# Kernel tuning notes

Measured on AMD Instinct MI355X. Metric: run time of the kernel, lower is better.

The kernel has to match this reference:

```python
import jax, jax.numpy as jnp
import numpy as np

N_ATOMS = 100000
M_NBRS = 12
ATOM_F = 64
NBR_F = 41
BN_EPS = 1e-5


def setup_inputs() -> dict:
    key = jax.random.key(0)
    k1, k2, k3, k4, k5 = jax.random.split(key, 5)
    atom_fea = jax.random.normal(k1, (N_ATOMS, ATOM_F), dtype=jnp.float32)
    nbr_fea = jax.random.normal(k2, (N_ATOMS, M_NBRS, NBR_F), dtype=jnp.float32)
    # fc_full: Linear(2*atom + nbr -> 2*atom), torch layout [out, in]
    in_dim = 2 * ATOM_F + NBR_F
    out_dim = 2 * ATOM_F
    W = jax.random.normal(k3, (out_dim, in_dim), dtype=jnp.float32) * (1.0 / np.sqrt(in_dim))
    b = jax.random.normal(k4, (out_dim,), dtype=jnp.float32) * 0.01
    gamma = jnp.ones((ATOM_F,), dtype=jnp.float32)
    beta = jnp.zeros((ATOM_F,), dtype=jnp.float32)
    nbr_idx = jax.random.randint(k5, (N_ATOMS, M_NBRS), 0, N_ATOMS, dtype=jnp.int32)
    return {"atom_fea": atom_fea, "nbr_fea": nbr_fea, "W": W, "b": b,
            "gamma": gamma, "beta": beta, "nbr_idx": nbr_idx}


def reference(atom_fea, nbr_fea, W, b, gamma, beta, nbr_idx):
    N, M = nbr_idx.shape
    F = atom_fea.shape[1]
    # gather neighbor atom features: [N, M, F]
    nbr_atom_fea = atom_fea[nbr_idx]
    # broadcast self features: [N, M, F]
    self_fea = jnp.broadcast_to(atom_fea[:, None, :], (N, M, F))
    # concat [self, nbr_atom, edge] -> [N, M, 2F + nbr_F]
    total_fea = jnp.concatenate([self_fea, nbr_atom_fea, nbr_fea], axis=2)
    # shared linear: [N, M, 2F]
    total_fea = jnp.einsum('nmi,oi->nmo', total_fea, W) + b
    filter_fea, core_fea = jnp.split(total_fea, 2, axis=2)
    # gated message, sum over neighbors -> [N, F]
    nbr_msg = (jax.nn.sigmoid(filter_fea) * jax.nn.softplus(core_fea)).sum(axis=1)
    # BatchNorm1d (training mode: batch stats, biased variance)
    x = atom_fea + nbr_msg
    mean = x.mean(axis=0)
    var = x.var(axis=0)
    x_hat = (x - mean) * jax.lax.rsqrt(var + BN_EPS)
    out = x_hat * gamma + beta
    return jax.nn.softplus(out)
```

## Files before the change

### kernel.cpp

```cpp
#include <hip/hip_runtime.h>

#define N_ATOMS 100000
#define M_NBRS 12
#define ATOM_F 64
#define NBR_F 41
#define OUT_DIM 128
#define IN_DIM 169
#define N_GROUPS (N_ATOMS / 16)
#define LOG2E 1.44269504f
#define LN2   0.69314718f

typedef __attribute__((ext_vector_type(8))) short short8;
typedef __attribute__((ext_vector_type(4))) float f32x4;
typedef __attribute__((ext_vector_type(4))) unsigned u32x4;

__device__ __forceinline__ unsigned cvt_pk(float a, float b) {
    unsigned r;
    asm("v_cvt_pk_bf16_f32 %0, %1, %2" : "=v"(r) : "v"(a), "v"(b));
    return r;
}
__device__ __forceinline__ float fexp2(float x) { return __builtin_amdgcn_exp2f(x); }
__device__ __forceinline__ float flog2(float x) { return __builtin_amdgcn_logf(x); }
__device__ __forceinline__ float frcp(float x)  { return __builtin_amdgcn_rcpf(x); }
__device__ __forceinline__ float softplus_f(float x) {
    return fmaxf(x, 0.f) + __logf(1.f + __expf(-fabsf(x)));
}

__global__ __launch_bounds__(256, 4) void k_prep(
    const float* __restrict__ atom, const float* __restrict__ W,
    const float* __restrict__ bias, unsigned* __restrict__ abf_u32,
    unsigned* __restrict__ A1P, float* __restrict__ SUM)
{
    __shared__ __align__(16) unsigned BFp[16 * 64 * 4];
    const int tid = threadIdx.x;
    const int w = tid >> 6, l = tid & 63;
    const int r = l & 15, g = l >> 4;

    if (blockIdx.x == 0 && tid < 128) SUM[tid] = 0.f;

    #pragma unroll
    for (int s = 0; s < 4; ++s) {
        int f = s * 4 + w;
        int nt = f >> 1, kk = f & 1;
        int col = nt * 16 + r;
        int kbase = kk * 32 + g * 8;
        const float* wp = W + col * IN_DIM + kbase;
        u32x4 pk;
        pk[0] = cvt_pk(wp[0] * LOG2E, wp[1] * LOG2E);
        pk[1] = cvt_pk(wp[2] * LOG2E, wp[3] * LOG2E);
        pk[2] = cvt_pk(wp[4] * LOG2E, wp[5] * LOG2E);
        pk[3] = cvt_pk(wp[6] * LOG2E, wp[7] * LOG2E);
        *reinterpret_cast<u32x4*>(&BFp[(f * 64 + l) * 4]) = pk;
    }
    __syncthreads();

    const int gw = blockIdx.x * 4 + w;
    if (gw >= N_GROUPS) return;
    const int base = gw * 16;

    float bb[8];
    #pragma unroll
    for (int nt = 0; nt < 8; ++nt) bb[nt] = bias[nt * 16 + r] * LOG2E;

    union { u32x4 u; short8 s; } af[2];
    #pragma unroll
    for (int kk = 0; kk < 2; ++kk) {
        const float4* ap = reinterpret_cast<const float4*>(atom)
                           + (size_t)(base + r) * 16 + kk * 8 + g * 2;
        float4 v0 = ap[0], v1 = ap[1];
        af[kk].u[0] = cvt_pk(v0.x, v0.y); af[kk].u[1] = cvt_pk(v0.z, v0.w);
        af[kk].u[2] = cvt_pk(v1.x, v1.y); af[kk].u[3] = cvt_pk(v1.z, v1.w);
        *reinterpret_cast<u32x4*>(&abf_u32[(size_t)(base + r) * 32 + kk * 16 + g * 4])
            = af[kk].u;
    }

    u32x4 outp[4];
    #pragma unroll
    for (int nt = 0; nt < 4; ++nt) {
        f32x4 accf = {0.f,0.f,0.f,0.f}, accc = {0.f,0.f,0.f,0.f};
        #pragma unroll
        for (int kk = 0; kk < 2; ++kk) {
            union { u32x4 u; short8 s; } uf, uc;
            uf.u = *reinterpret_cast<const u32x4*>(&BFp[((nt * 2 + kk) * 64 + l) * 4]);
            uc.u = *reinterpret_cast<const u32x4*>(&BFp[(((nt + 4) * 2 + kk) * 64 + l) * 4]);
            accf = __builtin_amdgcn_mfma_f32_16x16x32_bf16(af[kk].s, uf.s, accf, 0,0,0);
            accc = __builtin_amdgcn_mfma_f32_16x16x32_bf16(af[kk].s, uc.s, accc, 0,0,0);
        }
        #pragma unroll
        for (int r4 = 0; r4 < 4; ++r4)
            outp[r4][nt] = cvt_pk(accf[r4] + bb[nt], accc[r4] + bb[nt + 4]);
    }
    #pragma unroll
    for (int r4 = 0; r4 < 4; ++r4)
        *reinterpret_cast<u32x4*>(&A1P[(size_t)gw * 1024 + r4 * 256 + l * 4]) = outp[r4];
}

struct EBuf { unsigned p2[4]; unsigned p3[4]; };

__device__ __forceinline__ EBuf load_edges(const float* __restrict__ ep, int g)
{
    EBuf b;
    f32x4 v0, v1;
    __builtin_memcpy(&v0, ep + g * 8, 16);
    __builtin_memcpy(&v1, ep + g * 8 + 4, 16);
    b.p2[0] = cvt_pk(v0[0], v0[1]); b.p2[1] = cvt_pk(v0[2], v0[3]);
    b.p2[2] = cvt_pk(v1[0], v1[1]); b.p2[3] = cvt_pk(v1[2], v1[3]);
    b.p3[0] = b.p3[1] = b.p3[2] = b.p3[3] = 0u;
    if (g == 0) {
        f32x4 u0, u1;
        __builtin_memcpy(&u0, ep + 32, 16);
        __builtin_memcpy(&u1, ep + 36, 16);
        b.p3[0] = cvt_pk(u0[0], u0[1]); b.p3[1] = cvt_pk(u0[2], u0[3]);
        b.p3[2] = cvt_pk(u1[0], u1[1]); b.p3[3] = cvt_pk(u1[2], u1[3]);
    } else if (g == 1) {
        b.p3[0] = cvt_pk(ep[40], 0.f);
    }
    return b;
}

__global__ __launch_bounds__(256, 4) void k_msg(
    const float* __restrict__ atom, const float* __restrict__ nbr,
    const float* __restrict__ W, const int* __restrict__ idx,
    const unsigned* __restrict__ abf, const unsigned* __restrict__ A1P,
    float* __restrict__ X, float* __restrict__ SUM)
{
    __shared__ __align__(16) unsigned BF[32 * 64 * 4];
    const int tid = threadIdx.x;
    const int w = tid >> 6, l = tid & 63;
    const int c = l & 15, g = l >> 4;

    #pragma unroll
    for (int s = 0; s < 8; ++s) {
        int f = s * 4 + w;
        int nt = f >> 2, kk = f & 3;
        int col = nt * 16 + c;
        int kbase = kk * 32 + g * 8;
        const float* wp = W + col * IN_DIM + 64 + kbase;
        u32x4 pk;
        float v[8];
        #pragma unroll
        for (int j = 0; j < 8; ++j)
            v[j] = (kbase + j < 105) ? wp[j] * LOG2E : 0.f;
        pk[0] = cvt_pk(v[0], v[1]); pk[1] = cvt_pk(v[2], v[3]);
        pk[2] = cvt_pk(v[4], v[5]); pk[3] = cvt_pk(v[6], v[7]);
        *reinterpret_cast<u32x4*>(&BF[(f * 64 + l) * 4]) = pk;
    }
    __syncthreads();

    const int gw = blockIdx.x * 4 + w;
    float sum_p[4] = {0.f,0.f,0.f,0.f}, sq_p[4] = {0.f,0.f,0.f,0.f};

    if (gw < N_GROUPS) {
        const int base = gw * 16;
        u32x4 a1q[4];
        #pragma unroll
        for (int r4 = 0; r4 < 4; ++r4)
            a1q[r4] = *reinterpret_cast<const u32x4*>(
                &A1P[(size_t)gw * 1024 + r4 * 256 + l * 4]);

        float gs[4][4];
        #pragma unroll
        for (int r4 = 0; r4 < 4; ++r4)
          #pragma unroll
          for (int p = 0; p < 4; ++p) gs[r4][p] = 0.f;

        const int irow = (base + c) * M_NBRS;
        const float* erow = nbr + (size_t)irow * NBR_F;

        unsigned bofs = (unsigned)l * 16u;

        u32x4 at0, at1, at0n, at1n;
        EBuf eb, ebn;
        int jn;
        {
            int j0 = idx[irow];
            at0 = *reinterpret_cast<const u32x4*>(abf + (size_t)j0 * 32 + g * 4);
            at1 = *reinterpret_cast<const u32x4*>(abf + (size_t)j0 * 32 + 16 + g * 4);
            eb = load_edges(erow, g);
        }
        jn = idx[irow + 1];

        #pragma unroll 1
        for (int m = 0; m < M_NBRS; ++m) {
            if (m + 1 < M_NBRS) {
                at0n = *reinterpret_cast<const u32x4*>(abf + (size_t)jn * 32 + g * 4);
                at1n = *reinterpret_cast<const u32x4*>(abf + (size_t)jn * 32 + 16 + g * 4);
                ebn = load_edges(erow + (m + 1) * NBR_F, g);
                if (m + 2 < M_NBRS) jn = idx[irow + m + 2];
            }
            asm volatile("" : "+v"(bofs));
            const char* bsb = reinterpret_cast<const char*>(BF);
            union { u32x4 u; short8 s; } a0, a1, a2, a3;
            a0.u = at0; a1.u = at1;
            a2.u[0] = eb.p2[0]; a2.u[1] = eb.p2[1]; a2.u[2] = eb.p2[2]; a2.u[3] = eb.p2[3];
            a3.u[0] = eb.p3[0]; a3.u[1] = eb.p3[1]; a3.u[2] = eb.p3[2]; a3.u[3] = eb.p3[3];
            #pragma unroll
            for (int p = 0; p < 4; ++p) {
                f32x4 accf, accc;
                #pragma unroll
                for (int r4 = 0; r4 < 4; ++r4) {
                    unsigned v = a1q[r4][p];
                    accf[r4] = __uint_as_float(v << 16);
                    accc[r4] = __uint_as_float(v & 0xffff0000u);
                }
                #pragma unroll
                for (int kk = 0; kk < 4; ++kk) {
                    union { u32x4 u; short8 s; } uf, uc;
                    uf.u = *reinterpret_cast<const u32x4*>(
                        bsb + bofs + (unsigned)((p * 4 + kk) * 64 * 16));
                    uc.u = *reinterpret_cast<const u32x4*>(
                        bsb + bofs + (unsigned)(((p + 4) * 4 + kk) * 64 * 16));
                    short8 afk = (kk == 0) ? a0.s : (kk == 1) ? a1.s
                               : (kk == 2) ? a2.s : a3.s;
                    accf = __builtin_amdgcn_mfma_f32_16x16x32_bf16(afk, uf.s, accf, 0,0,0);
                    accc = __builtin_amdgcn_mfma_f32_16x16x32_bf16(afk, uc.s, accc, 0,0,0);
                }
                #pragma unroll
                for (int r4 = 0; r4 < 4; ++r4) {
                    float sig = frcp(1.f + fexp2(-accf[r4]));
                    float sp  = flog2(1.f + fexp2(accc[r4])) * LN2;
                    gs[r4][p] += sig * sp;
                }
            }
            at0 = at0n; at1 = at1n; eb = ebn;
        }
        #pragma unroll
        for (int r4 = 0; r4 < 4; ++r4) {
            int o = (base + g * 4 + r4) * ATOM_F + c;
            #pragma unroll
            for (int p = 0; p < 4; ++p) {
                float x = atom[o + p * 16] + gs[r4][p];
                X[o + p * 16] = x;
                sum_p[p] += x;
                sq_p[p] += x * x;
            }
        }
    }

    #pragma unroll
    for (int p = 0; p < 4; ++p) {
        sum_p[p] += __shfl_xor(sum_p[p], 16, 64);
        sum_p[p] += __shfl_xor(sum_p[p], 32, 64);
        sq_p[p]  += __shfl_xor(sq_p[p], 16, 64);
        sq_p[p]  += __shfl_xor(sq_p[p], 32, 64);
    }
    __syncthreads();
    float* Rs = reinterpret_cast<float*>(BF);
    if (g == 0) {
        #pragma unroll
        for (int p = 0; p < 4; ++p) {
            Rs[w * 128 + p * 16 + c] = sum_p[p];
            Rs[512 + w * 128 + p * 16 + c] = sq_p[p];
        }
    }
    __syncthreads();
    if (tid < 128) {
        int q = tid & 63;
        int o = (tid >> 6) * 512;
        float v = Rs[o + q] + Rs[o + 128 + q] + Rs[o + 256 + q] + Rs[o + 384 + q];
        atomicAdd(&SUM[tid], v);
    }
}

__global__ void k_final(float* __restrict__ X, const float* __restrict__ SUM,
                        const float* __restrict__ gamma, const float* __restrict__ beta)
{
    int q = blockIdx.x * 256 + threadIdx.x;
    int fb = (q & 15);
    const float4* S4 = reinterpret_cast<const float4*>(SUM);
    float4 s1 = S4[fb];
    float4 s2 = S4[16 + fb];
    float4 gm = reinterpret_cast<const float4*>(gamma)[fb];
    float4 bt = reinterpret_cast<const float4*>(beta)[fb];
    const float inv_n = 1.f / N_ATOMS;
    float4 x = reinterpret_cast<const float4*>(X)[q];
    float4 o;
    {
        float mean = s1.x * inv_n, msq = s2.x * inv_n;
        float sc = rsqrtf(msq - mean * mean + 1e-5f) * gm.x;
        o.x = softplus_f(x.x * sc + (bt.x - mean * sc));
    }
    {
        float mean = s1.y * inv_n, msq = s2.y * inv_n;
        float sc = rsqrtf(msq - mean * mean + 1e-5f) * gm.y;
        o.y = softplus_f(x.y * sc + (bt.y - mean * sc));
    }
    {
        float mean = s1.z * inv_n, msq = s2.z * inv_n;
        float sc = rsqrtf(msq - mean * mean + 1e-5f) * gm.z;
        o.z = softplus_f(x.z * sc + (bt.z - mean * sc));
    }
    {
        float mean = s1.w * inv_n, msq = s2.w * inv_n;
        float sc = rsqrtf(msq - mean * mean + 1e-5f) * gm.w;
        o.w = softplus_f(x.w * sc + (bt.w - mean * sc));
    }
    reinterpret_cast<float4*>(X)[q] = o;
}

extern "C" void kernel_launch(void* const* d_in, const int* in_sizes, int n_in,
                              void* d_out, int out_size, void* d_ws, size_t ws_size,
                              hipStream_t stream)
{
    const float* atom  = (const float*)d_in[0];
    const float* nbr   = (const float*)d_in[1];
    const float* W     = (const float*)d_in[2];
    const float* bias  = (const float*)d_in[3];
    const float* gamma = (const float*)d_in[4];
    const float* beta  = (const float*)d_in[5];
    const int*   idx   = (const int*)d_in[6];
    float* X = (float*)d_out;

    char* ws = (char*)d_ws;
    unsigned* abf = (unsigned*)ws;
    unsigned* A1P = (unsigned*)(ws + (size_t)N_ATOMS * 32 * 4);
    float* SUM    = (float*)(ws + (size_t)N_ATOMS * 32 * 4
                                + (size_t)N_GROUPS * 1024 * 4);

    const int blocks = (N_GROUPS + 3) / 4;
    hipLaunchKernelGGL(k_prep,  dim3(blocks), dim3(256), 0, stream, atom, W, bias, abf, A1P, SUM);
    hipLaunchKernelGGL(k_msg,   dim3(blocks), dim3(256), 0, stream, atom, nbr, W, idx, abf, A1P, X, SUM);
    hipLaunchKernelGGL(k_final, dim3(6250),   dim3(256), 0, stream, X, SUM, gamma, beta);
}
```

Baseline: 415.9 us.

## Pre-convert edge features to padded bf16 neighbor-major buffer in prep kernel

Moves the fp32-to-bf16 conversion of the edge features out of the message kernel into the prep kernel. The prep kernel writes them as 96-byte padded rows laid out neighbor-slab by atom, so the message loop fetches each operand with two aligned 16-byte loads instead of unaligned fp32 loads plus converts. The cost is an extra pass that reads all edge features (about 197 MB of fp32) and writes a roughly 115 MB bf16 buffer, which is then read again. Each thread in the prep pass also does strided 164-byte row reads, which coalesce poorly. Overall global traffic likely goes up.

```diff
diff --git a/kernel.cpp b/kernel.cpp
--- a/kernel.cpp
+++ b/kernel.cpp
@@ -27,9 +27,10 @@
 }
 
 __global__ __launch_bounds__(256, 4) void k_prep(
-    const float* __restrict__ atom, const float* __restrict__ W,
-    const float* __restrict__ bias, unsigned* __restrict__ abf_u32,
-    unsigned* __restrict__ A1P, float* __restrict__ SUM)
+    const float* __restrict__ atom, const float* __restrict__ nbr,
+    const float* __restrict__ W, const float* __restrict__ bias,
+    unsigned* __restrict__ abf_u32, unsigned* __restrict__ A1P,
+    unsigned* __restrict__ EP, float* __restrict__ SUM)
 {
     __shared__ __align__(16) unsigned BFp[16 * 64 * 4];
     const int tid = threadIdx.x;
@@ -54,6 +55,26 @@
     }
     __syncthreads();
 
+    {
+        const int tot = N_ATOMS * M_NBRS;
+        const int stride = gridDim.x * 256;
+        for (int T = blockIdx.x * 256 + tid; T < tot; T += stride) {
+            int m = T - (T / M_NBRS) * M_NBRS;
+            int a = T / M_NBRS;
+            const float* ip = nbr + (size_t)T * NBR_F;
+            unsigned o[24];
+            #pragma unroll
+            for (int u = 0; u < 20; ++u) o[u] = cvt_pk(ip[2 * u], ip[2 * u + 1]);
+            o[20] = cvt_pk(ip[40], 0.f);
+            o[21] = 0u; o[22] = 0u; o[23] = 0u;
+            unsigned* op = EP + ((size_t)m * N_ATOMS + a) * 24;
+            #pragma unroll
+            for (int q = 0; q < 6; ++q)
+                *reinterpret_cast<u32x4*>(op + q * 4) =
+                    *reinterpret_cast<const u32x4*>(&o[q * 4]);
+        }
+    }
+
     const int gw = blockIdx.x * 4 + w;
     if (gw >= N_GROUPS) return;
     const int base = gw * 16;
@@ -95,33 +116,10 @@
         *reinterpret_cast<u32x4*>(&A1P[(size_t)gw * 1024 + r4 * 256 + l * 4]) = outp[r4];
 }
 
-struct EBuf { unsigned p2[4]; unsigned p3[4]; };
-
-__device__ __forceinline__ EBuf load_edges(const float* __restrict__ ep, int g)
-{
-    EBuf b;
-    f32x4 v0, v1;
-    __builtin_memcpy(&v0, ep + g * 8, 16);
-    __builtin_memcpy(&v1, ep + g * 8 + 4, 16);
-    b.p2[0] = cvt_pk(v0[0], v0[1]); b.p2[1] = cvt_pk(v0[2], v0[3]);
-    b.p2[2] = cvt_pk(v1[0], v1[1]); b.p2[3] = cvt_pk(v1[2], v1[3]);
-    b.p3[0] = b.p3[1] = b.p3[2] = b.p3[3] = 0u;
-    if (g == 0) {
-        f32x4 u0, u1;
-        __builtin_memcpy(&u0, ep + 32, 16);
-        __builtin_memcpy(&u1, ep + 36, 16);
-        b.p3[0] = cvt_pk(u0[0], u0[1]); b.p3[1] = cvt_pk(u0[2], u0[3]);
-        b.p3[2] = cvt_pk(u1[0], u1[1]); b.p3[3] = cvt_pk(u1[2], u1[3]);
-    } else if (g == 1) {
-        b.p3[0] = cvt_pk(ep[40], 0.f);
-    }
-    return b;
-}
-
 __global__ __launch_bounds__(256, 4) void k_msg(
-    const float* __restrict__ atom, const float* __restrict__ nbr,
-    const float* __restrict__ W, const int* __restrict__ idx,
-    const unsigned* __restrict__ abf, const unsigned* __restrict__ A1P,
+    const float* __restrict__ atom, const float* __restrict__ W,
+    const int* __restrict__ idx, const unsigned* __restrict__ abf,
+    const unsigned* __restrict__ A1P, const unsigned* __restrict__ EP,
     float* __restrict__ X, float* __restrict__ SUM)
 {
     __shared__ __align__(16) unsigned BF[32 * 64 * 4];
@@ -165,18 +163,21 @@
           for (int p = 0; p < 4; ++p) gs[r4][p] = 0.f;
 
         const int irow = (base + c) * M_NBRS;
-        const float* erow = nbr + (size_t)irow * NBR_F;
+        const char* EPb = reinterpret_cast<const char*>(EP);
+        const size_t e2off = (size_t)(base + c) * 96 + (size_t)g * 16;
+        const size_t e3off = (size_t)(base + c) * 96 + 64 + (g == 1 ? 16 : 0);
+        const size_t slab = (size_t)N_ATOMS * 96;
 
         unsigned bofs = (unsigned)l * 16u;
 
-        u32x4 at0, at1, at0n, at1n;
-        EBuf eb, ebn;
+        u32x4 at0, at1, at0n, at1n, e2, e3, e2n, e3n;
         int jn;
         {
             int j0 = idx[irow];
             at0 = *reinterpret_cast<const u32x4*>(abf + (size_t)j0 * 32 + g * 4);
             at1 = *reinterpret_cast<const u32x4*>(abf + (size_t)j0 * 32 + 16 + g * 4);
-            eb = load_edges(erow, g);
+            e2 = *reinterpret_cast<const u32x4*>(EPb + e2off);
+            e3 = *reinterpret_cast<const u32x4*>(EPb + e3off);
         }
         jn = idx[irow + 1];
 
@@ -185,15 +186,14 @@
             if (m + 1 < M_NBRS) {
                 at0n = *reinterpret_cast<const u32x4*>(abf + (size_t)jn * 32 + g * 4);
                 at1n = *reinterpret_cast<const u32x4*>(abf + (size_t)jn * 32 + 16 + g * 4);
-                ebn = load_edges(erow + (m + 1) * NBR_F, g);
+                e2n = *reinterpret_cast<const u32x4*>(EPb + (m + 1) * slab + e2off);
+                e3n = *reinterpret_cast<const u32x4*>(EPb + (m + 1) * slab + e3off);
                 if (m + 2 < M_NBRS) jn = idx[irow + m + 2];
             }
             asm volatile("" : "+v"(bofs));
             const char* bsb = reinterpret_cast<const char*>(BF);
             union { u32x4 u; short8 s; } a0, a1, a2, a3;
-            a0.u = at0; a1.u = at1;
-            a2.u[0] = eb.p2[0]; a2.u[1] = eb.p2[1]; a2.u[2] = eb.p2[2]; a2.u[3] = eb.p2[3];
-            a3.u[0] = eb.p3[0]; a3.u[1] = eb.p3[1]; a3.u[2] = eb.p3[2]; a3.u[3] = eb.p3[3];
+            a0.u = at0; a1.u = at1; a2.u = e2; a3.u = e3;
             #pragma unroll
             for (int p = 0; p < 4; ++p) {
                 f32x4 accf, accc;
@@ -222,7 +222,7 @@
                     gs[r4][p] += sig * sp;
                 }
             }
-            at0 = at0n; at1 = at1n; eb = ebn;
+            at0 = at0n; at1 = at1n; e2 = e2n; e3 = e3n;
         }
         #pragma unroll
         for (int r4 = 0; r4 < 4; ++r4) {
@@ -314,11 +314,16 @@
     char* ws = (char*)d_ws;
     unsigned* abf = (unsigned*)ws;
     unsigned* A1P = (unsigned*)(ws + (size_t)N_ATOMS * 32 * 4);
+    unsigned* EP  = (unsigned*)(ws + (size_t)N_ATOMS * 32 * 4
+                                   + (size_t)N_GROUPS * 1024 * 4);
     float* SUM    = (float*)(ws + (size_t)N_ATOMS * 32 * 4
-                                + (size_t)N_GROUPS * 1024 * 4);
+                                + (size_t)N_GROUPS * 1024 * 4
+                                + (size_t)N_ATOMS * M_NBRS * 24 * 4);
 
     const int blocks = (N_GROUPS + 3) / 4;
-    hipLaunchKernelGGL(k_prep,  dim3(blocks), dim3(256), 0, stream, atom, W, bias, abf, A1P, SUM);
-    hipLaunchKernelGGL(k_msg,   dim3(blocks), dim3(256), 0, stream, atom, nbr, W, idx, abf, A1P, X, SUM);
+    hipLaunchKernelGGL(k_prep,  dim3(blocks), dim3(256), 0, stream,
+                       atom, nbr, W, bias, abf, A1P, EP, SUM);
+    hipLaunchKernelGGL(k_msg,   dim3(blocks), dim3(256), 0, stream,
+                       atom, W, idx, abf, A1P, EP, X, SUM);
     hipLaunchKernelGGL(k_final, dim3(6250),   dim3(256), 0, stream, X, SUM, gamma, beta);
 }
```

After: 450.9 us. +8.4%, slower.

## Fuse self-feature projection into message kernel and deepen edge prefetch

Applied to the files above, without the earlier changes.

Moves the self-atom half of the linear layer (the A1P precompute) out of the prep kernel and into the message kernel, which computes it with MFMA straight into registers. This removes the A1P workspace write and re-read. It also deepens the edge-feature prefetch to two neighbors ahead to hide more global load latency. The cost is an extra LDS weight staging pass and barrier in k_msg, plus higher register pressure from the extra edge buffer.

```diff
diff --git a/kernel.cpp b/kernel.cpp
--- a/kernel.cpp
+++ b/kernel.cpp
@@ -27,72 +27,29 @@
 }
 
 __global__ __launch_bounds__(256, 4) void k_prep(
-    const float* __restrict__ atom, const float* __restrict__ W,
-    const float* __restrict__ bias, unsigned* __restrict__ abf_u32,
-    unsigned* __restrict__ A1P, float* __restrict__ SUM)
-{
-    __shared__ __align__(16) unsigned BFp[16 * 64 * 4];
+    const float* __restrict__ atom, unsigned* __restrict__ abf_u32,
+    float* __restrict__ SUM)
+{
     const int tid = threadIdx.x;
     const int w = tid >> 6, l = tid & 63;
     const int r = l & 15, g = l >> 4;
 
     if (blockIdx.x == 0 && tid < 128) SUM[tid] = 0.f;
 
-    #pragma unroll
-    for (int s = 0; s < 4; ++s) {
-        int f = s * 4 + w;
-        int nt = f >> 1, kk = f & 1;
-        int col = nt * 16 + r;
-        int kbase = kk * 32 + g * 8;
-        const float* wp = W + col * IN_DIM + kbase;
-        u32x4 pk;
-        pk[0] = cvt_pk(wp[0] * LOG2E, wp[1] * LOG2E);
-        pk[1] = cvt_pk(wp[2] * LOG2E, wp[3] * LOG2E);
-        pk[2] = cvt_pk(wp[4] * LOG2E, wp[5] * LOG2E);
-        pk[3] = cvt_pk(wp[6] * LOG2E, wp[7] * LOG2E);
-        *reinterpret_cast<u32x4*>(&BFp[(f * 64 + l) * 4]) = pk;
-    }
-    __syncthreads();
-
     const int gw = blockIdx.x * 4 + w;
     if (gw >= N_GROUPS) return;
     const int base = gw * 16;
 
-    float bb[8];
-    #pragma unroll
-    for (int nt = 0; nt < 8; ++nt) bb[nt] = bias[nt * 16 + r] * LOG2E;
-
-    union { u32x4 u; short8 s; } af[2];
     #pragma unroll
     for (int kk = 0; kk < 2; ++kk) {
         const float4* ap = reinterpret_cast<const float4*>(atom)
                            + (size_t)(base + r) * 16 + kk * 8 + g * 2;
         float4 v0 = ap[0], v1 = ap[1];
-        af[kk].u[0] = cvt_pk(v0.x, v0.y); af[kk].u[1] = cvt_pk(v0.z, v0.w);
-        af[kk].u[2] = cvt_pk(v1.x, v1.y); af[kk].u[3] = cvt_pk(v1.z, v1.w);
-        *reinterpret_cast<u32x4*>(&abf_u32[(size_t)(base + r) * 32 + kk * 16 + g * 4])
-            = af[kk].u;
-    }
-
-    u32x4 outp[4];
-    #pragma unroll
-    for (int nt = 0; nt < 4; ++nt) {
-        f32x4 accf = {0.f,0.f,0.f,0.f}, accc = {0.f,0.f,0.f,0.f};
-        #pragma unroll
-        for (int kk = 0; kk < 2; ++kk) {
-            union { u32x4 u; short8 s; } uf, uc;
-            uf.u = *reinterpret_cast<const u32x4*>(&BFp[((nt * 2 + kk) * 64 + l) * 4]);
-            uc.u = *reinterpret_cast<const u32x4*>(&BFp[(((nt + 4) * 2 + kk) * 64 + l) * 4]);
-            accf = __builtin_amdgcn_mfma_f32_16x16x32_bf16(af[kk].s, uf.s, accf, 0,0,0);
-            accc = __builtin_amdgcn_mfma_f32_16x16x32_bf16(af[kk].s, uc.s, accc, 0,0,0);
-        }
-        #pragma unroll
-        for (int r4 = 0; r4 < 4; ++r4)
-            outp[r4][nt] = cvt_pk(accf[r4] + bb[nt], accc[r4] + bb[nt + 4]);
-    }
-    #pragma unroll
-    for (int r4 = 0; r4 < 4; ++r4)
-        *reinterpret_cast<u32x4*>(&A1P[(size_t)gw * 1024 + r4 * 256 + l * 4]) = outp[r4];
+        u32x4 u;
+        u[0] = cvt_pk(v0.x, v0.y); u[1] = cvt_pk(v0.z, v0.w);
+        u[2] = cvt_pk(v1.x, v1.y); u[3] = cvt_pk(v1.z, v1.w);
+        *reinterpret_cast<u32x4*>(&abf_u32[(size_t)(base + r) * 32 + kk * 16 + g * 4]) = u;
+    }
 }
 
 struct EBuf { unsigned p2[4]; unsigned p3[4]; };
@@ -120,14 +77,64 @@
 
 __global__ __launch_bounds__(256, 4) void k_msg(
     const float* __restrict__ atom, const float* __restrict__ nbr,
-    const float* __restrict__ W, const int* __restrict__ idx,
-    const unsigned* __restrict__ abf, const unsigned* __restrict__ A1P,
+    const float* __restrict__ W, const float* __restrict__ bias,
+    const int* __restrict__ idx, const unsigned* __restrict__ abf,
     float* __restrict__ X, float* __restrict__ SUM)
 {
     __shared__ __align__(16) unsigned BF[32 * 64 * 4];
     const int tid = threadIdx.x;
     const int w = tid >> 6, l = tid & 63;
     const int c = l & 15, g = l >> 4;
+
+    const int gw = blockIdx.x * 4 + w;
+    const bool active = (gw < N_GROUPS);
+    const int base = gw * 16;
+
+    #pragma unroll
+    for (int s = 0; s < 4; ++s) {
+        int f = s * 4 + w;
+        int nt = f >> 1, kk = f & 1;
+        int col = nt * 16 + c;
+        int kbase = kk * 32 + g * 8;
+        const float* wp = W + col * IN_DIM + kbase;
+        u32x4 pk;
+        pk[0] = cvt_pk(wp[0] * LOG2E, wp[1] * LOG2E);
+        pk[1] = cvt_pk(wp[2] * LOG2E, wp[3] * LOG2E);
+        pk[2] = cvt_pk(wp[4] * LOG2E, wp[5] * LOG2E);
+        pk[3] = cvt_pk(wp[6] * LOG2E, wp[7] * LOG2E);
+        *reinterpret_cast<u32x4*>(&BF[(f * 64 + l) * 4]) = pk;
+    }
+    __syncthreads();
+
+    u32x4 a1q[4];
+    #pragma unroll
+    for (int r4 = 0; r4 < 4; ++r4) a1q[r4] = u32x4{0u, 0u, 0u, 0u};
+    if (active) {
+        float bb[8];
+        #pragma unroll
+        for (int nt = 0; nt < 8; ++nt) bb[nt] = bias[nt * 16 + c] * LOG2E;
+        union { u32x4 u; short8 s; } af[2];
+        #pragma unroll
+        for (int kk = 0; kk < 2; ++kk)
+            af[kk].u = *reinterpret_cast<const u32x4*>(
+                &abf[(size_t)(base + c) * 32 + kk * 16 + g * 4]);
+        #pragma unroll
+        for (int nt = 0; nt < 4; ++nt) {
+            f32x4 accf = {0.f,0.f,0.f,0.f}, accc = {0.f,0.f,0.f,0.f};
+            #pragma unroll
+            for (int kk = 0; kk < 2; ++kk) {
+                union { u32x4 u; short8 s; } uf, uc;
+                uf.u = *reinterpret_cast<const u32x4*>(&BF[((nt * 2 + kk) * 64 + l) * 4]);
+                uc.u = *reinterpret_cast<const u32x4*>(&BF[(((nt + 4) * 2 + kk) * 64 + l) * 4]);
+                accf = __builtin_amdgcn_mfma_f32_16x16x32_bf16(af[kk].s, uf.s, accf, 0,0,0);
+                accc = __builtin_amdgcn_mfma_f32_16x16x32_bf16(af[kk].s, uc.s, accc, 0,0,0);
+            }
+            #pragma unroll
+            for (int r4 = 0; r4 < 4; ++r4)
+                a1q[r4][nt] = cvt_pk(accf[r4] + bb[nt], accc[r4] + bb[nt + 4]);
+        }
+    }
+    __syncthreads();
 
     #pragma unroll
     for (int s = 0; s < 8; ++s) {
@@ -147,17 +154,9 @@
     }
     __syncthreads();
 
-    const int gw = blockIdx.x * 4 + w;
     float sum_p[4] = {0.f,0.f,0.f,0.f}, sq_p[4] = {0.f,0.f,0.f,0.f};
 
-    if (gw < N_GROUPS) {
-        const int base = gw * 16;
-        u32x4 a1q[4];
-        #pragma unroll
-        for (int r4 = 0; r4 < 4; ++r4)
-            a1q[r4] = *reinterpret_cast<const u32x4*>(
-                &A1P[(size_t)gw * 1024 + r4 * 256 + l * 4]);
-
+    if (active) {
         float gs[4][4];
         #pragma unroll
         for (int r4 = 0; r4 < 4; ++r4)
@@ -170,13 +169,14 @@
         unsigned bofs = (unsigned)l * 16u;
 
         u32x4 at0, at1, at0n, at1n;
-        EBuf eb, ebn;
+        EBuf eb, ebn, eb2;
         int jn;
         {
             int j0 = idx[irow];
             at0 = *reinterpret_cast<const u32x4*>(abf + (size_t)j0 * 32 + g * 4);
             at1 = *reinterpret_cast<const u32x4*>(abf + (size_t)j0 * 32 + 16 + g * 4);
-            eb = load_edges(erow, g);
+            eb  = load_edges(erow, g);
+            ebn = load_edges(erow + NBR_F, g);
         }
         jn = idx[irow + 1];
 
@@ -185,9 +185,10 @@
             if (m + 1 < M_NBRS) {
                 at0n = *reinterpret_cast<const u32x4*>(abf + (size_t)jn * 32 + g * 4);
                 at1n = *reinterpret_cast<const u32x4*>(abf + (size_t)jn * 32 + 16 + g * 4);
-                ebn = load_edges(erow + (m + 1) * NBR_F, g);
                 if (m + 2 < M_NBRS) jn = idx[irow + m + 2];
             }
+            if (m + 2 < M_NBRS)
+                eb2 = load_edges(erow + (m + 2) * NBR_F, g);
             asm volatile("" : "+v"(bofs));
             const char* bsb = reinterpret_cast<const char*>(BF);
             union { u32x4 u; short8 s; } a0, a1, a2, a3;
@@ -222,7 +223,7 @@
                     gs[r4][p] += sig * sp;
                 }
             }
-            at0 = at0n; at1 = at1n; eb = ebn;
+            at0 = at0n; at1 = at1n; eb = ebn; ebn = eb2;
         }
         #pragma unroll
         for (int r4 = 0; r4 < 4; ++r4) {
@@ -313,12 +314,11 @@
 
     char* ws = (char*)d_ws;
     unsigned* abf = (unsigned*)ws;
-    unsigned* A1P = (unsigned*)(ws + (size_t)N_ATOMS * 32 * 4);
-    float* SUM    = (float*)(ws + (size_t)N_ATOMS * 32 * 4
-                                + (size_t)N_GROUPS * 1024 * 4);
+    float* SUM    = (float*)(ws + (size_t)N_ATOMS * 32 * 4);
 
     const int blocks = (N_GROUPS + 3) / 4;
-    hipLaunchKernelGGL(k_prep,  dim3(blocks), dim3(256), 0, stream, atom, W, bias, abf, A1P, SUM);
-    hipLaunchKernelGGL(k_msg,   dim3(blocks), dim3(256), 0, stream, atom, nbr, W, idx, abf, A1P, X, SUM);
+    hipLaunchKernelGGL(k_prep,  dim3(blocks), dim3(256), 0, stream, atom, abf, SUM);
+    hipLaunchKernelGGL(k_msg,   dim3(blocks), dim3(256), 0, stream,
+                       atom, nbr, W, bias, idx, abf, X, SUM);
     hipLaunchKernelGGL(k_final, dim3(6250),   dim3(256), 0, stream, X, SUM, gamma, beta);
 }
```

Result: slower. 437.3 us (+5.1%).
